# Kernel optimization log

Hardware: AMD Instinct MI355X
Metric: run time of the kernel (lower is better)

## Reference

```python
import jax, jax.numpy as jnp
import numpy as np

EPS = 1e-5

def _layernorm(x, gamma, beta):
    # LayerNormalization over last axis (channels), epsilon=1e-5
    mu = jnp.mean(x, axis=-1, keepdims=True)
    var = jnp.var(x, axis=-1, keepdims=True)
    return (x - mu) * jax.lax.rsqrt(var + EPS) * gamma + beta

def setup_inputs() -> dict:
    key = jax.random.key(0)
    ks = jax.random.split(key, 6)
    B, H, W, C = 8, 64, 64, 256
    std = 0.1  # NIN init_scale
    return {
        "x": jax.random.normal(ks[0], (B, H, W, C), dtype=jnp.float32),
        "ln_gamma": jnp.ones((C,), dtype=jnp.float32),
        "ln_beta": jnp.zeros((C,), dtype=jnp.float32),
        "wq": jax.random.normal(ks[1], (C, C), dtype=jnp.float32) * std,
        "bq": jnp.zeros((C,), dtype=jnp.float32),
        "wk": jax.random.normal(ks[2], (C, C), dtype=jnp.float32) * std,
        "bk": jnp.zeros((C,), dtype=jnp.float32),
        "wv": jax.random.normal(ks[3], (C, C), dtype=jnp.float32) * std,
        "bv": jnp.zeros((C,), dtype=jnp.float32),
        "wo": jax.random.normal(ks[4], (C, C), dtype=jnp.float32) * std,
        "bo": jnp.zeros((C,), dtype=jnp.float32),
    }

def reference(x, ln_gamma, ln_beta, wq, bq, wk, bk, wv, bv, wo, bo):
    B, H, W, C = x.shape
    h = _layernorm(x, ln_gamma, ln_beta)
    # 1x1 convs == per-pixel channel matmuls
    q = jnp.einsum('bhwc,cd->bhwd', h, wq) + bq
    k = jnp.einsum('bhwc,cd->bhwd', h, wk) + bk
    v = jnp.einsum('bhwc,cd->bhwd', h, wv) + bv
    scale = jnp.float32(C) ** -0.5
    # dense spatial attention over all H*W tokens
    w = jnp.einsum('bhwc,bijc->bhwij', q, k) * scale  # [B,H,W,H,W]
    w = jax.nn.softmax(w.reshape(B, H, W, H * W), axis=-1).reshape(B, H, W, H, W)
    h = jnp.einsum('bhwij,bijc->bhwc', w, v)
    h = jnp.einsum('bhwc,cd->bhwd', h, wo) + bo
    return x + h
```

## Files before the change

kernel.cpp:

```cpp
#include <hip/hip_runtime.h>
#include <stdint.h>

#define NB    8
#define NTOK  4096
#define TOK   32768
#define CDIM  256
#define BQ    128
#define BK    64
#define NT    (NTOK / BK)

#define KPITCH 264
#define VPITCH 68
#define KTILE_SH (BK * KPITCH)
#define VTILE_SH (CDIM * VPITCH)
#define KCH   33
#define VCH   34
#define TOTCH (KCH + VCH)

typedef __attribute__((ext_vector_type(8))) short bf16x8;
typedef __attribute__((ext_vector_type(4))) float f32x4;

#define SSCALE 0.09016844f

static __device__ __forceinline__ unsigned short f2bf(float f) {
    union { float f; unsigned u; } v; v.f = f;
    unsigned r = v.u + 0x7fffu + ((v.u >> 16) & 1u);
    return (unsigned short)(r >> 16);
}

static __device__ __forceinline__ void dma16(const unsigned short* g, unsigned short* l) {
    __builtin_amdgcn_global_load_lds(
        (const __attribute__((address_space(1))) unsigned int*)g,
        (__attribute__((address_space(3))) unsigned int*)l,
        16, 0, 0);
}

__global__ __launch_bounds__(256) void prep_kernel(
        const float* __restrict__ x,
        const float* __restrict__ gamma,
        const float* __restrict__ beta,
        const float* __restrict__ w0, const float* __restrict__ w1,
        const float* __restrict__ w2, const float* __restrict__ w3,
        unsigned short* __restrict__ h_bf,
        unsigned short* __restrict__ wt) {
    int bx = blockIdx.x;
    if (bx >= TOK / 4) {
        int id = bx - TOK / 4;
        int m = id >> 8, dd = id & 255;
        const float* src = (m == 0) ? w0 : (m == 1) ? w1 : (m == 2) ? w2 : w3;
        wt[m * (CDIM * CDIM) + dd * CDIM + threadIdx.x] = f2bf(src[threadIdx.x * CDIM + dd]);
        return;
    }
    int w = threadIdx.x >> 6;
    int lane = threadIdx.x & 63;
    int token = bx * 4 + w;
    const float4 xv = ((const float4*)(x + (size_t)token * CDIM))[lane];
    float s = xv.x + xv.y + xv.z + xv.w;
    #pragma unroll
    for (int off = 1; off < 64; off <<= 1) s += __shfl_xor(s, off, 64);
    float mean = s * (1.0f / 256.0f);
    float d0 = xv.x - mean, d1 = xv.y - mean, d2 = xv.z - mean, d3 = xv.w - mean;
    float ss = d0 * d0 + d1 * d1 + d2 * d2 + d3 * d3;
    #pragma unroll
    for (int off = 1; off < 64; off <<= 1) ss += __shfl_xor(ss, off, 64);
    float rstd = rsqrtf(ss * (1.0f / 256.0f) + 1e-5f);
    float4 g = ((const float4*)gamma)[lane];
    float4 b = ((const float4*)beta)[lane];
    ushort4 o;
    o.x = f2bf(d0 * rstd * g.x + b.x);
    o.y = f2bf(d1 * rstd * g.y + b.y);
    o.z = f2bf(d2 * rstd * g.z + b.z);
    o.w = f2bf(d3 * rstd * g.w + b.w);
    ((ushort4*)(h_bf + (size_t)token * CDIM))[lane] = o;
}

__global__ __launch_bounds__(128) void qkv_kernel(
        const unsigned short* __restrict__ h_bf,
        const unsigned short* __restrict__ wts,
        const float* __restrict__ bq,
        const float* __restrict__ bk,
        const float* __restrict__ bv,
        unsigned short* __restrict__ q_bf,
        unsigned short* __restrict__ k2,
        unsigned short* __restrict__ vt2) {
    __shared__ unsigned short VT[64][VPITCH];
    int tid = threadIdx.x;
    int w = tid >> 6, lane = tid & 63, quad = lane >> 4, l16 = lane & 15;
    int blk = blockIdx.x;
    int gy = blockIdx.y;
    int nt0 = gy * 4;
    int tok_base = blk * 64 + w * 32;

    bf16x8 afr[2][8];
    #pragma unroll
    for (int s = 0; s < 2; ++s)
        #pragma unroll
        for (int kk = 0; kk < 8; ++kk)
            afr[s][kk] = *(const bf16x8*)(h_bf + (size_t)(tok_base + s * 16 + l16) * CDIM + kk * 32 + quad * 8);

    {
        const unsigned short* wq_t = wts;
        #pragma unroll
        for (int ntl = 0; ntl < 4; ++ntl) {
            int nt = nt0 + ntl;
            f32x4 acc0 = {0.f, 0.f, 0.f, 0.f};
            f32x4 acc1 = {0.f, 0.f, 0.f, 0.f};
            #pragma unroll
            for (int kk = 0; kk < 8; ++kk) {
                bf16x8 bfr = *(const bf16x8*)(wq_t + (size_t)(nt * 16 + l16) * CDIM + kk * 32 + quad * 8);
                acc0 = __builtin_amdgcn_mfma_f32_16x16x32_bf16(bfr, afr[0][kk], acc0, 0, 0, 0);
                acc1 = __builtin_amdgcn_mfma_f32_16x16x32_bf16(bfr, afr[1][kk], acc1, 0, 0, 0);
            }
            int d0 = nt * 16 + quad * 4;
            float4 b4 = *(const float4*)(bq + d0);
            ushort4 o0, o1;
            o0.x = f2bf((acc0[0] + b4.x) * SSCALE); o0.y = f2bf((acc0[1] + b4.y) * SSCALE);
            o0.z = f2bf((acc0[2] + b4.z) * SSCALE); o0.w = f2bf((acc0[3] + b4.w) * SSCALE);
            o1.x = f2bf((acc1[0] + b4.x) * SSCALE); o1.y = f2bf((acc1[1] + b4.y) * SSCALE);
            o1.z = f2bf((acc1[2] + b4.z) * SSCALE); o1.w = f2bf((acc1[3] + b4.w) * SSCALE);
            *(ushort4*)(q_bf + (size_t)(tok_base + l16) * CDIM + d0)      = o0;
            *(ushort4*)(q_bf + (size_t)(tok_base + 16 + l16) * CDIM + d0) = o1;
        }
    }
    {
        const unsigned short* wk_t = wts + CDIM * CDIM;
        unsigned short* kdst = k2 + (size_t)blk * KTILE_SH;
        int key0 = w * 32 + l16;
        #pragma unroll
        for (int ntl = 0; ntl < 4; ++ntl) {
            int nt = nt0 + ntl;
            f32x4 acc0 = {0.f, 0.f, 0.f, 0.f};
            f32x4 acc1 = {0.f, 0.f, 0.f, 0.f};
            #pragma unroll
            for (int kk = 0; kk < 8; ++kk) {
                bf16x8 bfr = *(const bf16x8*)(wk_t + (size_t)(nt * 16 + l16) * CDIM + kk * 32 + quad * 8);
                acc0 = __builtin_amdgcn_mfma_f32_16x16x32_bf16(bfr, afr[0][kk], acc0, 0, 0, 0);
                acc1 = __builtin_amdgcn_mfma_f32_16x16x32_bf16(bfr, afr[1][kk], acc1, 0, 0, 0);
            }
            int d0 = nt * 16 + quad * 4;
            float4 b4 = *(const float4*)(bk + d0);
            ushort4 o0, o1;
            o0.x = f2bf(acc0[0] + b4.x); o0.y = f2bf(acc0[1] + b4.y);
            o0.z = f2bf(acc0[2] + b4.z); o0.w = f2bf(acc0[3] + b4.w);
            o1.x = f2bf(acc1[0] + b4.x); o1.y = f2bf(acc1[1] + b4.y);
            o1.z = f2bf(acc1[2] + b4.z); o1.w = f2bf(acc1[3] + b4.w);
            *(ushort4*)(kdst + (size_t)key0 * KPITCH + d0)        = o0;
            *(ushort4*)(kdst + (size_t)(key0 + 16) * KPITCH + d0) = o1;
        }
    }
    {
        const unsigned short* wv_t = wts + 2 * CDIM * CDIM;
        #pragma unroll
        for (int ntl = 0; ntl < 4; ++ntl) {
            int nt = nt0 + ntl;
            f32x4 acc0 = {0.f, 0.f, 0.f, 0.f};
            f32x4 acc1 = {0.f, 0.f, 0.f, 0.f};
            #pragma unroll
            for (int kk = 0; kk < 8; ++kk) {
                bf16x8 bfr = *(const bf16x8*)(wv_t + (size_t)(nt * 16 + l16) * CDIM + kk * 32 + quad * 8);
                acc0 = __builtin_amdgcn_mfma_f32_16x16x32_bf16(afr[0][kk], bfr, acc0, 0, 0, 0);
                acc1 = __builtin_amdgcn_mfma_f32_16x16x32_bf16(afr[1][kk], bfr, acc1, 0, 0, 0);
            }
            int d = nt * 16 + l16;
            float bb = bv[d];
            int dl = ntl * 16 + l16;
            #pragma unroll
            for (int r = 0; r < 4; ++r) {
                VT[dl][w * 32 + quad * 8 + r]     = f2bf(acc0[r] + bb);
                VT[dl][w * 32 + quad * 8 + 4 + r] = f2bf(acc1[r] + bb);
            }
        }
    }
    __syncthreads();
    const uint4* src = (const uint4*)(&VT[0][0]);
    uint4* dst = (uint4*)(vt2 + (size_t)blk * VTILE_SH + (size_t)gy * 64 * VPITCH);
    #pragma unroll
    for (int i = 0; i < 4; ++i)
        dst[i * 128 + tid] = src[i * 128 + tid];
    if (tid < 32) dst[512 + tid] = src[512 + tid];
}

#define DMA_TILE(KS, VS, ktn)                                                        \
    {                                                                                \
        const unsigned short* gk = k2 + (size_t)(b * NT + (ktn)) * KTILE_SH;         \
        const unsigned short* gv = vt2 + (size_t)(b * NT + (ktn)) * VTILE_SH;        \
        for (int c = w; c < TOTCH; c += 8) {                                         \
            if (c < KCH) dma16(gk + c * 512 + lane * 8, &KS[0][0] + c * 512);        \
            else dma16(gv + (c - KCH) * 512 + lane * 8, &VS[0][0] + (c - KCH) * 512);\
        }                                                                            \
    }

#define WAIT_TILE() asm volatile("s_waitcnt vmcnt(8)\n\ts_barrier" ::: "memory");
#define WAIT_ALL()  asm volatile("s_waitcnt vmcnt(0)\n\ts_barrier" ::: "memory");
#define READ_DONE() asm volatile("s_waitcnt lgkmcnt(0)\n\ts_barrier" ::: "memory");

#define COMPUTE_TILE(KS, VS)                                                         \
    {                                                                                \
        f32x4 sfr[2][2];                                                             \
        _Pragma("unroll")                                                            \
        for (int nt = 0; nt < 2; ++nt) {                                             \
            f32x4 a0 = {0.f, 0.f, 0.f, 0.f};                                         \
            f32x4 a1 = {0.f, 0.f, 0.f, 0.f};                                         \
            _Pragma("unroll")                                                        \
            for (int kk = 0; kk < 8; ++kk) {                                         \
                bf16x8 kb = *(const bf16x8*)(&KS[kh * 32 + nt * 16 + l16][kk * 32 + quad * 8]); \
                a0 = __builtin_amdgcn_mfma_f32_16x16x32_bf16(kb, qfr[0][kk], a0, 0, 0, 0);      \
                a1 = __builtin_amdgcn_mfma_f32_16x16x32_bf16(kb, qfr[1][kk], a1, 0, 0, 0);      \
            }                                                                        \
            sfr[0][nt] = a0; sfr[1][nt] = a1;                                        \
        }                                                                            \
        int4 pwv[2];                                                                 \
        _Pragma("unroll")                                                            \
        for (int s = 0; s < 2; ++s) {                                                \
            unsigned pw[4];                                                          \
            _Pragma("unroll")                                                        \
            for (int nt = 0; nt < 2; ++nt)                                           \
                _Pragma("unroll")                                                    \
                for (int h = 0; h < 2; ++h) {                                        \
                    float plo = exp2f(sfr[s][nt][2 * h]);                            \
                    float phi = exp2f(sfr[s][nt][2 * h + 1]);                        \
                    lacc[s] += plo + phi;                                            \
                    pw[nt * 2 + h] = (__float_as_uint(plo) >> 16)                    \
                                   | (__float_as_uint(phi) & 0xffff0000u);           \
                }                                                                    \
            pwv[s] = make_int4(pw[0], pw[1], pw[2], pw[3]);                          \
        }                                                                            \
        bf16x8 pfr0 = *(bf16x8*)&pwv[0];                                             \
        bf16x8 pfr1 = *(bf16x8*)&pwv[1];                                             \
        _Pragma("unroll")                                                            \
        for (int nt2 = 0; nt2 < 16; ++nt2) {                                         \
            bf16x8 vb = *(const bf16x8*)(&VS[nt2 * 16 + l16][kh * 32 + quad * 8]);   \
            O[0][nt2] = __builtin_amdgcn_mfma_f32_16x16x32_bf16(pfr0, vb, O[0][nt2], 0, 0, 0);  \
            O[1][nt2] = __builtin_amdgcn_mfma_f32_16x16x32_bf16(pfr1, vb, O[1][nt2], 0, 0, 0);  \
        }                                                                            \
    }

__global__ __launch_bounds__(512, 2) void flash_kernel(
        const unsigned short* __restrict__ q_bf,
        const unsigned short* __restrict__ k2,
        const unsigned short* __restrict__ vt2,
        unsigned short* __restrict__ attn) {
    __shared__ unsigned short Ks0[BK][KPITCH];
    __shared__ unsigned short Ks1[BK][KPITCH];
    __shared__ unsigned short Vs0[CDIM][VPITCH];
    __shared__ unsigned short Vs1[CDIM][VPITCH];
    __shared__ float sLbuf[512];

    int tid = threadIdx.x;
    int w = tid >> 6, lane = tid & 63, quad = lane >> 4, l16 = lane & 15;
    int kh = w >> 2;
    int wq = w & 3;
    int bid = blockIdx.x;
    int b = bid & 7;
    int qtile = bid >> 3;
    int qrow = qtile * BQ + wq * 32;
    const size_t bbase = (size_t)b * NTOK * CDIM;

    bf16x8 qfr[2][8];
    #pragma unroll
    for (int s = 0; s < 2; ++s)
        #pragma unroll
        for (int kk = 0; kk < 8; ++kk)
            qfr[s][kk] = *(const bf16x8*)(q_bf + bbase + (size_t)(qrow + s * 16 + l16) * CDIM + kk * 32 + quad * 8);

    f32x4 O[2][16];
    #pragma unroll
    for (int s = 0; s < 2; ++s)
        #pragma unroll
        for (int i = 0; i < 16; ++i) O[s][i] = (f32x4){0.f, 0.f, 0.f, 0.f};
    float lacc[2] = {0.f, 0.f};

    DMA_TILE(Ks0, Vs0, 0);

    for (int kt2 = 0; kt2 < NT; kt2 += 2) {
        DMA_TILE(Ks1, Vs1, kt2 + 1);
        WAIT_TILE()
        COMPUTE_TILE(Ks0, Vs0);
        READ_DONE()
        if (kt2 + 2 < NT) {
            DMA_TILE(Ks0, Vs0, kt2 + 2);
            WAIT_TILE()
        } else {
            WAIT_ALL()
        }
        COMPUTE_TILE(Ks1, Vs1);
        READ_DONE()
    }

    float* sO = (wq == 0) ? (float*)&Ks0[0][0] : (wq == 1) ? (float*)&Ks1[0][0]
              : (wq == 2) ? (float*)&Vs0[0][0] : (float*)&Vs1[0][0];
    float* sL = sLbuf + wq * 128;

    if (kh == 1) {
        #pragma unroll
        for (int s = 0; s < 2; ++s) {
            #pragma unroll
            for (int nt2 = 0; nt2 < 16; ++nt2)
                #pragma unroll
                for (int r = 0; r < 4; ++r)
                    sO[((s * 16 + nt2) * 4 + r) * 64 + lane] = O[s][nt2][r];
            sL[s * 64 + lane] = lacc[s];
        }
    }
    __syncthreads();
    if (kh == 0) {
        float lr[2][4];
        #pragma unroll
        for (int s = 0; s < 2; ++s) {
            float ls = lacc[s] + sL[s * 64 + lane];
            ls += __shfl_xor(ls, 16, 64);
            ls += __shfl_xor(ls, 32, 64);
            float li = 1.0f / ls;
            #pragma unroll
            for (int r = 0; r < 4; ++r)
                lr[s][r] = __shfl(li, quad * 4 + r, 64);
        }
        #pragma unroll
        for (int s = 0; s < 2; ++s)
            #pragma unroll
            for (int nt2 = 0; nt2 < 16; ++nt2) {
                int d = nt2 * 16 + l16;
                #pragma unroll
                for (int r = 0; r < 4; ++r) {
                    float val = (O[s][nt2][r] + sO[((s * 16 + nt2) * 4 + r) * 64 + lane]) * lr[s][r];
                    attn[bbase + (size_t)(qrow + s * 16 + quad * 4 + r) * CDIM + d] = f2bf(val);
                }
            }
    }
}

__global__ __launch_bounds__(128) void oproj_kernel(
        const unsigned short* __restrict__ attn,
        const unsigned short* __restrict__ wo_t,
        const float* __restrict__ bo,
        const float* __restrict__ x,
        float* __restrict__ out) {
    int w = threadIdx.x >> 6, lane = threadIdx.x & 63;
    int quad = lane >> 4, l16 = lane & 15;
    int tok_base = blockIdx.x * 64 + w * 32;
    int nt0 = blockIdx.y * 8;

    bf16x8 afr[2][8];
    #pragma unroll
    for (int s = 0; s < 2; ++s)
        #pragma unroll
        for (int kk = 0; kk < 8; ++kk)
            afr[s][kk] = *(const bf16x8*)(attn + (size_t)(tok_base + s * 16 + l16) * CDIM + kk * 32 + quad * 8);

    #pragma unroll
    for (int ntl = 0; ntl < 8; ++ntl) {
        int nt = nt0 + ntl;
        f32x4 acc0 = {0.f, 0.f, 0.f, 0.f};
        f32x4 acc1 = {0.f, 0.f, 0.f, 0.f};
        #pragma unroll
        for (int kk = 0; kk < 8; ++kk) {
            bf16x8 bfr = *(const bf16x8*)(wo_t + (size_t)(nt * 16 + l16) * CDIM + kk * 32 + quad * 8);
            acc0 = __builtin_amdgcn_mfma_f32_16x16x32_bf16(bfr, afr[0][kk], acc0, 0, 0, 0);
            acc1 = __builtin_amdgcn_mfma_f32_16x16x32_bf16(bfr, afr[1][kk], acc1, 0, 0, 0);
        }
        int d0 = nt * 16 + quad * 4;
        float4 b4 = *(const float4*)(bo + d0);
        size_t i0 = (size_t)(tok_base + l16) * CDIM + d0;
        size_t i1 = (size_t)(tok_base + 16 + l16) * CDIM + d0;
        float4 x0 = *(const float4*)(x + i0);
        float4 x1 = *(const float4*)(x + i1);
        float4 o0, o1;
        o0.x = x0.x + acc0[0] + b4.x; o0.y = x0.y + acc0[1] + b4.y;
        o0.z = x0.z + acc0[2] + b4.z; o0.w = x0.w + acc0[3] + b4.w;
        o1.x = x1.x + acc1[0] + b4.x; o1.y = x1.y + acc1[1] + b4.y;
        o1.z = x1.z + acc1[2] + b4.z; o1.w = x1.w + acc1[3] + b4.w;
        *(float4*)(out + i0) = o0;
        *(float4*)(out + i1) = o1;
    }
}

extern "C" void kernel_launch(void* const* d_in, const int* in_sizes, int n_in,
                              void* d_out, int out_size, void* d_ws, size_t ws_size,
                              hipStream_t stream) {
    const float* x     = (const float*)d_in[0];
    const float* gamma = (const float*)d_in[1];
    const float* beta  = (const float*)d_in[2];
    const float* wq    = (const float*)d_in[3];
    const float* bq    = (const float*)d_in[4];
    const float* wk    = (const float*)d_in[5];
    const float* bk    = (const float*)d_in[6];
    const float* wv    = (const float*)d_in[7];
    const float* bv    = (const float*)d_in[8];
    const float* wo    = (const float*)d_in[9];
    const float* bo    = (const float*)d_in[10];
    float* out = (float*)d_out;

    char* ws = (char*)d_ws;
    unsigned short* h_bf = (unsigned short*)(ws);
    unsigned short* q_bf = (unsigned short*)(ws + 16777216);
    unsigned short* k2   = (unsigned short*)(ws + 33554432);
    unsigned short* vt2  = (unsigned short*)(ws + 50855936);
    unsigned short* wt   = (unsigned short*)(ws + 68681728);
    unsigned short* attn = h_bf;

    prep_kernel<<<TOK / 4 + 1024, 256, 0, stream>>>(x, gamma, beta, wq, wk, wv, wo, h_bf, wt);
    qkv_kernel<<<dim3(TOK / 64, 4), 128, 0, stream>>>(h_bf, wt, bq, bk, bv, q_bf, k2, vt2);
    flash_kernel<<<(NTOK / BQ) * NB, 512, 0, stream>>>(q_bf, k2, vt2, attn);
    oproj_kernel<<<dim3(TOK / 64, 2), 128, 0, stream>>>(attn, wt + 3 * (CDIM * CDIM), bo, x, out);
}
```

Measured before the change: 366.4 us.

## Fuse output projection and residual into flash attention epilogue

Moves the Wo projection, bias and residual add into the flash kernel epilogue. The normalized attention tile is staged as bf16 in shared memory, so the separate oproj launch and the global attn round-trip go away. Shared memory becomes one flat buffer with pointer aliases. The explicit vmcnt-based waits in the double-buffered loop are replaced by plain __syncthreads, which may reduce load/compute overlap or depend on compiler-inserted waits for the LDS DMA.

```diff
diff --git a/kernel.cpp b/kernel.cpp
--- a/kernel.cpp
+++ b/kernel.cpp
@@ -16,6 +16,8 @@
 #define KCH   33
 #define VCH   34
 #define TOTCH (KCH + VCH)
+
+#define APITCH 264
 
 typedef __attribute__((ext_vector_type(8))) short bf16x8;
 typedef __attribute__((ext_vector_type(4))) float f32x4;
@@ -180,21 +182,17 @@
     if (tid < 32) dst[512 + tid] = src[512 + tid];
 }
 
-#define DMA_TILE(KS, VS, ktn)                                                        \
+#define DMA_TILE(KSp, VSp, ktn)                                                      \
     {                                                                                \
         const unsigned short* gk = k2 + (size_t)(b * NT + (ktn)) * KTILE_SH;         \
         const unsigned short* gv = vt2 + (size_t)(b * NT + (ktn)) * VTILE_SH;        \
         for (int c = w; c < TOTCH; c += 8) {                                         \
-            if (c < KCH) dma16(gk + c * 512 + lane * 8, &KS[0][0] + c * 512);        \
-            else dma16(gv + (c - KCH) * 512 + lane * 8, &VS[0][0] + (c - KCH) * 512);\
+            if (c < KCH) dma16(gk + c * 512 + lane * 8, (KSp) + c * 512);            \
+            else dma16(gv + (c - KCH) * 512 + lane * 8, (VSp) + (c - KCH) * 512);    \
         }                                                                            \
     }
 
-#define WAIT_TILE() asm volatile("s_waitcnt vmcnt(8)\n\ts_barrier" ::: "memory");
-#define WAIT_ALL()  asm volatile("s_waitcnt vmcnt(0)\n\ts_barrier" ::: "memory");
-#define READ_DONE() asm volatile("s_waitcnt lgkmcnt(0)\n\ts_barrier" ::: "memory");
-
-#define COMPUTE_TILE(KS, VS)                                                         \
+#define COMPUTE_TILE(KSp, VSp)                                                       \
     {                                                                                \
         f32x4 sfr[2][2];                                                             \
         _Pragma("unroll")                                                            \
@@ -203,7 +201,9 @@
             f32x4 a1 = {0.f, 0.f, 0.f, 0.f};                                         \
             _Pragma("unroll")                                                        \
             for (int kk = 0; kk < 8; ++kk) {                                         \
-                bf16x8 kb = *(const bf16x8*)(&KS[kh * 32 + nt * 16 + l16][kk * 32 + quad * 8]); \
+                bf16x8 kb = *(const bf16x8*)((KSp)                                   \
+                    + (size_t)(kh * 32 + nt * 16 + l16) * KPITCH                     \
+                    + kk * 32 + quad * 8);                                           \
                 a0 = __builtin_amdgcn_mfma_f32_16x16x32_bf16(kb, qfr[0][kk], a0, 0, 0, 0);      \
                 a1 = __builtin_amdgcn_mfma_f32_16x16x32_bf16(kb, qfr[1][kk], a1, 0, 0, 0);      \
             }                                                                        \
@@ -229,7 +229,8 @@
         bf16x8 pfr1 = *(bf16x8*)&pwv[1];                                             \
         _Pragma("unroll")                                                            \
         for (int nt2 = 0; nt2 < 16; ++nt2) {                                         \
-            bf16x8 vb = *(const bf16x8*)(&VS[nt2 * 16 + l16][kh * 32 + quad * 8]);   \
+            bf16x8 vb = *(const bf16x8*)((VSp)                                       \
+                + (size_t)(nt2 * 16 + l16) * VPITCH + kh * 32 + quad * 8);           \
             O[0][nt2] = __builtin_amdgcn_mfma_f32_16x16x32_bf16(pfr0, vb, O[0][nt2], 0, 0, 0);  \
             O[1][nt2] = __builtin_amdgcn_mfma_f32_16x16x32_bf16(pfr1, vb, O[1][nt2], 0, 0, 0);  \
         }                                                                            \
@@ -239,12 +240,16 @@
         const unsigned short* __restrict__ q_bf,
         const unsigned short* __restrict__ k2,
         const unsigned short* __restrict__ vt2,
-        unsigned short* __restrict__ attn) {
-    __shared__ unsigned short Ks0[BK][KPITCH];
-    __shared__ unsigned short Ks1[BK][KPITCH];
-    __shared__ unsigned short Vs0[CDIM][VPITCH];
-    __shared__ unsigned short Vs1[CDIM][VPITCH];
-    __shared__ float sLbuf[512];
+        const unsigned short* __restrict__ wo_t,
+        const float* __restrict__ bo,
+        const float* __restrict__ x,
+        float* __restrict__ out) {
+    __shared__ unsigned short SMEM[69632];
+    unsigned short* KS0 = SMEM;
+    unsigned short* KS1 = SMEM + 16896;
+    unsigned short* VS0 = SMEM + 33792;
+    unsigned short* VS1 = SMEM + 51200;
+    float* SL = (float*)(SMEM + 68608);
 
     int tid = threadIdx.x;
     int w = tid >> 6, lane = tid & 63, quad = lane >> 4, l16 = lane & 15;
@@ -270,26 +275,20 @@
         for (int i = 0; i < 16; ++i) O[s][i] = (f32x4){0.f, 0.f, 0.f, 0.f};
     float lacc[2] = {0.f, 0.f};
 
-    DMA_TILE(Ks0, Vs0, 0);
+    DMA_TILE(KS0, VS0, 0);
+    __syncthreads();
 
     for (int kt2 = 0; kt2 < NT; kt2 += 2) {
-        DMA_TILE(Ks1, Vs1, kt2 + 1);
-        WAIT_TILE()
-        COMPUTE_TILE(Ks0, Vs0);
-        READ_DONE()
-        if (kt2 + 2 < NT) {
-            DMA_TILE(Ks0, Vs0, kt2 + 2);
-            WAIT_TILE()
-        } else {
-            WAIT_ALL()
-        }
-        COMPUTE_TILE(Ks1, Vs1);
-        READ_DONE()
-    }
-
-    float* sO = (wq == 0) ? (float*)&Ks0[0][0] : (wq == 1) ? (float*)&Ks1[0][0]
-              : (wq == 2) ? (float*)&Vs0[0][0] : (float*)&Vs1[0][0];
-    float* sL = sLbuf + wq * 128;
+        DMA_TILE(KS1, VS1, kt2 + 1);
+        COMPUTE_TILE(KS0, VS0);
+        __syncthreads();
+        if (kt2 + 2 < NT) DMA_TILE(KS0, VS0, kt2 + 2);
+        COMPUTE_TILE(KS1, VS1);
+        __syncthreads();
+    }
+
+    float* sO = (float*)((wq == 0) ? KS0 : (wq == 1) ? KS1 : (wq == 2) ? VS0 : VS1);
+    float* sL = SL + wq * 128;
 
     if (kh == 1) {
         #pragma unroll
@@ -318,59 +317,48 @@
         #pragma unroll
         for (int s = 0; s < 2; ++s)
             #pragma unroll
-            for (int nt2 = 0; nt2 < 16; ++nt2) {
-                int d = nt2 * 16 + l16;
+            for (int nt2 = 0; nt2 < 16; ++nt2)
                 #pragma unroll
-                for (int r = 0; r < 4; ++r) {
-                    float val = (O[s][nt2][r] + sO[((s * 16 + nt2) * 4 + r) * 64 + lane]) * lr[s][r];
-                    attn[bbase + (size_t)(qrow + s * 16 + quad * 4 + r) * CDIM + d] = f2bf(val);
-                }
-            }
-    }
-}
-
-__global__ __launch_bounds__(128) void oproj_kernel(
-        const unsigned short* __restrict__ attn,
-        const unsigned short* __restrict__ wo_t,
-        const float* __restrict__ bo,
-        const float* __restrict__ x,
-        float* __restrict__ out) {
-    int w = threadIdx.x >> 6, lane = threadIdx.x & 63;
-    int quad = lane >> 4, l16 = lane & 15;
-    int tok_base = blockIdx.x * 64 + w * 32;
-    int nt0 = blockIdx.y * 8;
-
-    bf16x8 afr[2][8];
-    #pragma unroll
-    for (int s = 0; s < 2; ++s)
+                for (int r = 0; r < 4; ++r)
+                    O[s][nt2][r] = (O[s][nt2][r] + sO[((s * 16 + nt2) * 4 + r) * 64 + lane]) * lr[s][r];
+    }
+    __syncthreads();
+
+    if (kh == 0) {
+        #pragma unroll
+        for (int s = 0; s < 2; ++s)
+            #pragma unroll
+            for (int nt2 = 0; nt2 < 16; ++nt2)
+                #pragma unroll
+                for (int r = 0; r < 4; ++r)
+                    SMEM[(wq * 32 + s * 16 + quad * 4 + r) * APITCH + nt2 * 16 + l16]
+                        = f2bf(O[s][nt2][r]);
+    }
+    __syncthreads();
+
+    {
+        bf16x8 afr2[8];
         #pragma unroll
         for (int kk = 0; kk < 8; ++kk)
-            afr[s][kk] = *(const bf16x8*)(attn + (size_t)(tok_base + s * 16 + l16) * CDIM + kk * 32 + quad * 8);
-
-    #pragma unroll
-    for (int ntl = 0; ntl < 8; ++ntl) {
-        int nt = nt0 + ntl;
-        f32x4 acc0 = {0.f, 0.f, 0.f, 0.f};
-        f32x4 acc1 = {0.f, 0.f, 0.f, 0.f};
-        #pragma unroll
-        for (int kk = 0; kk < 8; ++kk) {
-            bf16x8 bfr = *(const bf16x8*)(wo_t + (size_t)(nt * 16 + l16) * CDIM + kk * 32 + quad * 8);
-            acc0 = __builtin_amdgcn_mfma_f32_16x16x32_bf16(bfr, afr[0][kk], acc0, 0, 0, 0);
-            acc1 = __builtin_amdgcn_mfma_f32_16x16x32_bf16(bfr, afr[1][kk], acc1, 0, 0, 0);
-        }
-        int d0 = nt * 16 + quad * 4;
-        float4 b4 = *(const float4*)(bo + d0);
-        size_t i0 = (size_t)(tok_base + l16) * CDIM + d0;
-        size_t i1 = (size_t)(tok_base + 16 + l16) * CDIM + d0;
-        float4 x0 = *(const float4*)(x + i0);
-        float4 x1 = *(const float4*)(x + i1);
-        float4 o0, o1;
-        o0.x = x0.x + acc0[0] + b4.x; o0.y = x0.y + acc0[1] + b4.y;
-        o0.z = x0.z + acc0[2] + b4.z; o0.w = x0.w + acc0[3] + b4.w;
-        o1.x = x1.x + acc1[0] + b4.x; o1.y = x1.y + acc1[1] + b4.y;
-        o1.z = x1.z + acc1[2] + b4.z; o1.w = x1.w + acc1[3] + b4.w;
-        *(float4*)(out + i0) = o0;
-        *(float4*)(out + i1) = o1;
+            afr2[kk] = *(const bf16x8*)(SMEM + (w * 16 + l16) * APITCH + kk * 32 + quad * 8);
+        int tokg = qtile * BQ + w * 16;
+        #pragma unroll
+        for (int nt = 0; nt < 16; ++nt) {
+            f32x4 acc = {0.f, 0.f, 0.f, 0.f};
+            #pragma unroll
+            for (int kk = 0; kk < 8; ++kk) {
+                bf16x8 bfr = *(const bf16x8*)(wo_t + (size_t)(nt * 16 + l16) * CDIM + kk * 32 + quad * 8);
+                acc = __builtin_amdgcn_mfma_f32_16x16x32_bf16(bfr, afr2[kk], acc, 0, 0, 0);
+            }
+            int d0 = nt * 16 + quad * 4;
+            float4 b4 = *(const float4*)(bo + d0);
+            size_t idx = bbase + (size_t)(tokg + l16) * CDIM + d0;
+            float4 x4 = *(const float4*)(x + idx);
+            float4 o4;
+            o4.x = x4.x + acc[0] + b4.x; o4.y = x4.y + acc[1] + b4.y;
+            o4.z = x4.z + acc[2] + b4.z; o4.w = x4.w + acc[3] + b4.w;
+            *(float4*)(out + idx) = o4;
+        }
     }
 }
 
@@ -396,10 +384,9 @@
     unsigned short* k2   = (unsigned short*)(ws + 33554432);
     unsigned short* vt2  = (unsigned short*)(ws + 50855936);
     unsigned short* wt   = (unsigned short*)(ws + 68681728);
-    unsigned short* attn = h_bf;
 
     prep_kernel<<<TOK / 4 + 1024, 256, 0, stream>>>(x, gamma, beta, wq, wk, wv, wo, h_bf, wt);
     qkv_kernel<<<dim3(TOK / 64, 4), 128, 0, stream>>>(h_bf, wt, bq, bk, bv, q_bf, k2, vt2);
-    flash_kernel<<<(NTOK / BQ) * NB, 512, 0, stream>>>(q_bf, k2, vt2, attn);
-    oproj_kernel<<<dim3(TOK / 64, 2), 128, 0, stream>>>(attn, wt + 3 * (CDIM * CDIM), bo, x, out);
-}
+    flash_kernel<<<(NTOK / BQ) * NB, 512, 0, stream>>>(
+        q_bf, k2, vt2, wt + 3 * (CDIM * CDIM), bo, x, out);
+}
```

Result: slower. 523.8 us (+43.0%).

## Fuse output projection into flash attention epilogue and simplify tile synchronisation

Applied to the files above, without the earlier changes.

Merges the output projection and residual add into the end of the flash attention kernel. The normalised bf16 attention tile is staged in shared memory, and each of the 8 waves multiplies it by its own 32 columns of Wo, then writes x + h + bias directly. This removes the separate oproj launch and the global round trip of the attention tensor. It also replaces the hand-written vmcnt/lgkmcnt waits with plain __syncthreads, which may stop the DMA of the next tile from overlapping with compute. The output stores are scalar and strided per lane rather than float4, so write coalescing may be worse.

```diff
diff --git a/kernel.cpp b/kernel.cpp
--- a/kernel.cpp
+++ b/kernel.cpp
@@ -189,10 +189,6 @@
             else dma16(gv + (c - KCH) * 512 + lane * 8, &VS[0][0] + (c - KCH) * 512);\
         }                                                                            \
     }
-
-#define WAIT_TILE() asm volatile("s_waitcnt vmcnt(8)\n\ts_barrier" ::: "memory");
-#define WAIT_ALL()  asm volatile("s_waitcnt vmcnt(0)\n\ts_barrier" ::: "memory");
-#define READ_DONE() asm volatile("s_waitcnt lgkmcnt(0)\n\ts_barrier" ::: "memory");
 
 #define COMPUTE_TILE(KS, VS)                                                         \
     {                                                                                \
@@ -239,7 +235,10 @@
         const unsigned short* __restrict__ q_bf,
         const unsigned short* __restrict__ k2,
         const unsigned short* __restrict__ vt2,
-        unsigned short* __restrict__ attn) {
+        const unsigned short* __restrict__ wo_t,
+        const float* __restrict__ bo,
+        const float* __restrict__ x,
+        float* __restrict__ out) {
     __shared__ unsigned short Ks0[BK][KPITCH];
     __shared__ unsigned short Ks1[BK][KPITCH];
     __shared__ unsigned short Vs0[CDIM][VPITCH];
@@ -271,20 +270,15 @@
     float lacc[2] = {0.f, 0.f};
 
     DMA_TILE(Ks0, Vs0, 0);
+    __syncthreads();
 
     for (int kt2 = 0; kt2 < NT; kt2 += 2) {
         DMA_TILE(Ks1, Vs1, kt2 + 1);
-        WAIT_TILE()
         COMPUTE_TILE(Ks0, Vs0);
-        READ_DONE()
-        if (kt2 + 2 < NT) {
-            DMA_TILE(Ks0, Vs0, kt2 + 2);
-            WAIT_TILE()
-        } else {
-            WAIT_ALL()
-        }
+        __syncthreads();
+        if (kt2 + 2 < NT) DMA_TILE(Ks0, Vs0, kt2 + 2);
         COMPUTE_TILE(Ks1, Vs1);
-        READ_DONE()
+        __syncthreads();
     }
 
     float* sO = (wq == 0) ? (float*)&Ks0[0][0] : (wq == 1) ? (float*)&Ks1[0][0]
@@ -318,59 +312,68 @@
         #pragma unroll
         for (int s = 0; s < 2; ++s)
             #pragma unroll
-            for (int nt2 = 0; nt2 < 16; ++nt2) {
-                int d = nt2 * 16 + l16;
+            for (int nt2 = 0; nt2 < 16; ++nt2)
                 #pragma unroll
-                for (int r = 0; r < 4; ++r) {
-                    float val = (O[s][nt2][r] + sO[((s * 16 + nt2) * 4 + r) * 64 + lane]) * lr[s][r];
-                    attn[bbase + (size_t)(qrow + s * 16 + quad * 4 + r) * CDIM + d] = f2bf(val);
-                }
-            }
-    }
-}
-
-__global__ __launch_bounds__(128) void oproj_kernel(
-        const unsigned short* __restrict__ attn,
-        const unsigned short* __restrict__ wo_t,
-        const float* __restrict__ bo,
-        const float* __restrict__ x,
-        float* __restrict__ out) {
-    int w = threadIdx.x >> 6, lane = threadIdx.x & 63;
-    int quad = lane >> 4, l16 = lane & 15;
-    int tok_base = blockIdx.x * 64 + w * 32;
-    int nt0 = blockIdx.y * 8;
-
-    bf16x8 afr[2][8];
-    #pragma unroll
-    for (int s = 0; s < 2; ++s)
-        #pragma unroll
-        for (int kk = 0; kk < 8; ++kk)
-            afr[s][kk] = *(const bf16x8*)(attn + (size_t)(tok_base + s * 16 + l16) * CDIM + kk * 32 + quad * 8);
-
-    #pragma unroll
-    for (int ntl = 0; ntl < 8; ++ntl) {
-        int nt = nt0 + ntl;
-        f32x4 acc0 = {0.f, 0.f, 0.f, 0.f};
-        f32x4 acc1 = {0.f, 0.f, 0.f, 0.f};
-        #pragma unroll
-        for (int kk = 0; kk < 8; ++kk) {
-            bf16x8 bfr = *(const bf16x8*)(wo_t + (size_t)(nt * 16 + l16) * CDIM + kk * 32 + quad * 8);
-            acc0 = __builtin_amdgcn_mfma_f32_16x16x32_bf16(bfr, afr[0][kk], acc0, 0, 0, 0);
-            acc1 = __builtin_amdgcn_mfma_f32_16x16x32_bf16(bfr, afr[1][kk], acc1, 0, 0, 0);
-        }
-        int d0 = nt * 16 + quad * 4;
-        float4 b4 = *(const float4*)(bo + d0);
-        size_t i0 = (size_t)(tok_base + l16) * CDIM + d0;
-        size_t i1 = (size_t)(tok_base + 16 + l16) * CDIM + d0;
-        float4 x0 = *(const float4*)(x + i0);
-        float4 x1 = *(const float4*)(x + i1);
-        float4 o0, o1;
-        o0.x = x0.x + acc0[0] + b4.x; o0.y = x0.y + acc0[1] + b4.y;
-        o0.z = x0.z + acc0[2] + b4.z; o0.w = x0.w + acc0[3] + b4.w;
-        o1.x = x1.x + acc1[0] + b4.x; o1.y = x1.y + acc1[1] + b4.y;
-        o1.z = x1.z + acc1[2] + b4.z; o1.w = x1.w + acc1[3] + b4.w;
-        *(float4*)(out + i0) = o0;
-        *(float4*)(out + i1) = o1;
+                for (int r = 0; r < 4; ++r)
+                    O[s][nt2][r] = (O[s][nt2][r] + sO[((s * 16 + nt2) * 4 + r) * 64 + lane]) * lr[s][r];
+    }
+    __syncthreads();
+
+    if (kh == 0) {
+        if (wq < 2) {
+            #pragma unroll
+            for (int s = 0; s < 2; ++s)
+                #pragma unroll
+                for (int nt2 = 0; nt2 < 16; ++nt2)
+                    #pragma unroll
+                    for (int r = 0; r < 4; ++r)
+                        Ks0[(wq & 1) * 32 + s * 16 + quad * 4 + r][nt2 * 16 + l16] = f2bf(O[s][nt2][r]);
+        } else {
+            #pragma unroll
+            for (int s = 0; s < 2; ++s)
+                #pragma unroll
+                for (int nt2 = 0; nt2 < 16; ++nt2)
+                    #pragma unroll
+                    for (int r = 0; r < 4; ++r)
+                        Ks1[(wq & 1) * 32 + s * 16 + quad * 4 + r][nt2 * 16 + l16] = f2bf(O[s][nt2][r]);
+        }
+    }
+    __syncthreads();
+
+    {
+        bf16x8 wfr[2][8];
+        #pragma unroll
+        for (int t = 0; t < 2; ++t)
+            #pragma unroll
+            for (int kk = 0; kk < 8; ++kk)
+                wfr[t][kk] = *(const bf16x8*)(wo_t + (size_t)((w * 2 + t) * 16 + l16) * CDIM + kk * 32 + quad * 8);
+        float bb0 = bo[(w * 2 + 0) * 16 + l16];
+        float bb1 = bo[(w * 2 + 1) * 16 + l16];
+        int tok0 = qtile * BQ;
+        #pragma unroll
+        for (int rg = 0; rg < 8; ++rg) {
+            bf16x8 afr2[8];
+            #pragma unroll
+            for (int kk = 0; kk < 8; ++kk)
+                afr2[kk] = (rg < 4)
+                    ? *(const bf16x8*)(&Ks0[rg * 16 + l16][kk * 32 + quad * 8])
+                    : *(const bf16x8*)(&Ks1[(rg - 4) * 16 + l16][kk * 32 + quad * 8]);
+            f32x4 acc0 = {0.f, 0.f, 0.f, 0.f};
+            f32x4 acc1 = {0.f, 0.f, 0.f, 0.f};
+            #pragma unroll
+            for (int kk = 0; kk < 8; ++kk) {
+                acc0 = __builtin_amdgcn_mfma_f32_16x16x32_bf16(afr2[kk], wfr[0][kk], acc0, 0, 0, 0);
+                acc1 = __builtin_amdgcn_mfma_f32_16x16x32_bf16(afr2[kk], wfr[1][kk], acc1, 0, 0, 0);
+            }
+            #pragma unroll
+            for (int r = 0; r < 4; ++r) {
+                size_t idx = bbase + (size_t)(tok0 + rg * 16 + quad * 4 + r) * CDIM;
+                size_t i0 = idx + (w * 2 + 0) * 16 + l16;
+                size_t i1 = idx + (w * 2 + 1) * 16 + l16;
+                out[i0] = x[i0] + acc0[r] + bb0;
+                out[i1] = x[i1] + acc1[r] + bb1;
+            }
+        }
     }
 }
 
@@ -396,10 +399,9 @@
     unsigned short* k2   = (unsigned short*)(ws + 33554432);
     unsigned short* vt2  = (unsigned short*)(ws + 50855936);
     unsigned short* wt   = (unsigned short*)(ws + 68681728);
-    unsigned short* attn = h_bf;
 
     prep_kernel<<<TOK / 4 + 1024, 256, 0, stream>>>(x, gamma, beta, wq, wk, wv, wo, h_bf, wt);
     qkv_kernel<<<dim3(TOK / 64, 4), 128, 0, stream>>>(h_bf, wt, bq, bk, bv, q_bf, k2, vt2);
-    flash_kernel<<<(NTOK / BQ) * NB, 512, 0, stream>>>(q_bf, k2, vt2, attn);
-    oproj_kernel<<<dim3(TOK / 64, 2), 128, 0, stream>>>(attn, wt + 3 * (CDIM * CDIM), bo, x, out);
-}
+    flash_kernel<<<(NTOK / BQ) * NB, 512, 0, stream>>>(
+        q_bf, k2, vt2, wt + 3 * (CDIM * CDIM), bo, x, out);
+}
```

Result: faster. 339.6 us (-7.3%).
